# Optimization experiments

Measured on AMD Instinct MI355X. Metric: run time of the kernel, lower is better.

## Reference

```python
import jax, jax.numpy as jnp
import numpy as np

N = 100_000      # nodes
E = 1_600_000    # edges (avg degree 16)
F_IN = 128       # input features
H = 64           # hidden
C = 40           # classes


def setup_inputs() -> dict:
    key = jax.random.key(0)
    ks = jax.random.split(key, 12)
    s = 0.05
    return {
        "x": jax.random.normal(ks[0], (N, F_IN), dtype=jnp.float32),
        "edge_index": jax.random.randint(ks[1], (2, E), 0, N, dtype=jnp.int64),
        "edge_weight": jax.random.uniform(ks[2], (E,), dtype=jnp.float32),
        # first_lin: Linear(F_IN, H)
        "W_first": jax.random.normal(ks[3], (F_IN, H), dtype=jnp.float32) * s,
        "b_first": jnp.zeros((H,), jnp.float32),
        # convs[0], convs[1]: GCNConv(H, H)
        "W_c1": jax.random.normal(ks[4], (H, H), dtype=jnp.float32) * s,
        "b_c1": jnp.zeros((H,), jnp.float32),
        "W_c2": jax.random.normal(ks[5], (H, H), dtype=jnp.float32) * s,
        "b_c2": jnp.zeros((H,), jnp.float32),
        # lin2: Linear(H, C)
        "W_out": jax.random.normal(ks[6], (H, C), dtype=jnp.float32) * s,
        "b_out": jnp.zeros((C,), jnp.float32),
    }


def gcn_conv(h, edge_weight, row, col, W, b, n):
    """PyG GCNConv: h' = D^-1/2 (A + I) D^-1/2 (h W) + b, with edge weights."""
    h = h @ W                                        # [n, H]
    # add self-loops with weight 1
    loops = jnp.arange(n, dtype=row.dtype)
    row_sl = jnp.concatenate([row, loops])           # source nodes
    col_sl = jnp.concatenate([col, loops])           # target nodes
    ew_sl = jnp.concatenate([edge_weight, jnp.ones((n,), edge_weight.dtype)])
    # symmetric normalization
    deg = jax.ops.segment_sum(ew_sl, col_sl, num_segments=n)
    dinv = jnp.where(deg > 0, jax.lax.rsqrt(jnp.where(deg > 0, deg, 1.0)), 0.0)
    norm = dinv[row_sl] * ew_sl * dinv[col_sl]       # [E+n]
    # gather -> scale -> scatter-add at targets
    msgs = norm[:, None] * h[row_sl]                 # [E+n, H]
    out = jax.ops.segment_sum(msgs, col_sl, num_segments=n)
    return out + b


def reference(x, edge_index, edge_weight, W_first, b_first, W_c1, b_c1,
              W_c2, b_c2, W_out, b_out):
    row, col = edge_index[0], edge_index[1]
    n = x.shape[0]
    h = jax.nn.relu(x @ W_first + b_first)           # first_lin + relu (dropout eval no-op)
    h = jax.nn.relu(gcn_conv(h, edge_weight, row, col, W_c1, b_c1, n))
    h = jax.nn.relu(gcn_conv(h, edge_weight, row, col, W_c2, b_c2, n))
    logits = h @ W_out + b_out                       # lin2
    return jax.nn.log_softmax(logits, axis=-1)
```

## Files before the change

### kernel.cpp

```cpp
#include <hip/hip_runtime.h>
#include <hip/hip_bf16.h>
#include <cstdint>
#include <cstddef>

#define NN 100000
#define NE 1600000
#define FIN 128
#define HD 64
#define NC 40
#define NTILE (NN / 16)
#define MM_BLOCKS ((NTILE + 3) / 4)

#define BUK 256
#define NBUK ((NN + BUK - 1) / BUK)
#define EPB 1024
#define NBLK ((NE + EPB - 1) / EPB)

#define XSTR 68
#define HSTR 36

typedef unsigned short u16;
typedef unsigned int u32;
typedef __attribute__((ext_vector_type(8))) short short8v;
typedef __attribute__((ext_vector_type(4))) float accf4;
typedef __attribute__((ext_vector_type(2))) float f32x2;

__device__ __forceinline__ float u2lo(u32 u) { return __uint_as_float(u << 16); }
__device__ __forceinline__ float u2hi(u32 u) { return __uint_as_float(u & 0xFFFF0000u); }
__device__ __forceinline__ u16 f2b(float f) {
    u32 u = __float_as_uint(f);
    return (u16)((u + 0x7FFFu + ((u >> 16) & 1u)) >> 16);
}
__device__ __forceinline__ u32 pk2(float lo, float hi) {
    return (u32)f2b(lo) | ((u32)f2b(hi) << 16);
}
__device__ __forceinline__ unsigned char f2fp8(float v) {
    int r = __builtin_amdgcn_cvt_pk_fp8_f32(v, 0.f, 0, false);
    return (unsigned char)(r & 0xFF);
}

__launch_bounds__(256)
__global__ void k_build1(const int* __restrict__ ei, u32* __restrict__ hist,
                         const float* __restrict__ x, const float* __restrict__ W,
                         const float* __restrict__ b, u16* __restrict__ out) {
    if (blockIdx.x < NBLK) {
        __shared__ u32 lh[NBUK];
        int blk = blockIdx.x, tid = threadIdx.x;
        for (int i = tid; i < NBUK; i += 256) lh[i] = 0;
        __syncthreads();
        #pragma unroll
        for (int it = 0; it < EPB / 256; it++) {
            int e = blk * EPB + it * 256 + tid;
            if (e < NE) {
                int col = ei[NE + e];
                atomicAdd(&lh[col >> 8], 1u);
            }
        }
        __syncthreads();
        for (int i = tid; i < NBUK; i += 256)
            hist[(size_t)blk * NBUK + i] = lh[i];
        return;
    }
    __shared__ u32 xs[64 * XSTR];
    int tid = threadIdx.x;
    int bi  = blockIdx.x - NBLK;
    int nodeB = bi * 64;
    const float4* x4 = (const float4*)x;
    for (int idx = tid; idx < 64 * 16; idx += 256) {
        int row = idx >> 4, seg = idx & 15;
        uint4 d = make_uint4(0u, 0u, 0u, 0u);
        if (nodeB + row < NN) {
            float4 a = x4[(size_t)(nodeB + row) * 32 + seg * 2];
            float4 c = x4[(size_t)(nodeB + row) * 32 + seg * 2 + 1];
            d.x = pk2(a.x, a.y);
            d.y = pk2(a.z, a.w);
            d.z = pk2(c.x, c.y);
            d.w = pk2(c.z, c.w);
        }
        *(uint4*)(xs + row * XSTR + seg * 4) = d;
    }
    __syncthreads();
    int lane = tid & 63;
    int wv   = tid >> 6;
    int tile = bi * 4 + wv;
    if (tile >= NTILE) return;
    int row = lane & 15;
    int kg  = lane >> 4;
    short8v bW[4][4];
    #pragma unroll
    for (int kt = 0; kt < 4; kt++)
        #pragma unroll
        for (int ct = 0; ct < 4; ct++)
            #pragma unroll
            for (int j = 0; j < 8; j++)
                bW[kt][ct][j] = (short)f2b(W[(kt*32 + kg*8 + j) * HD + ct*16 + row]);
    int node0 = tile * 16;
    short8v af[4];
    #pragma unroll
    for (int kt = 0; kt < 4; kt++)
        af[kt] = *(const short8v*)(xs + (wv*16 + row) * XSTR + kt * 16 + kg * 4);
    accf4 acc[4] = {};
    #pragma unroll
    for (int kt = 0; kt < 4; kt++)
        #pragma unroll
        for (int ct = 0; ct < 4; ct++)
            acc[ct] = __builtin_amdgcn_mfma_f32_16x16x32_bf16(af[kt], bW[kt][ct], acc[ct], 0, 0, 0);
    #pragma unroll
    for (int ct = 0; ct < 4; ct++) {
        float bias = b[ct*16 + row];
        #pragma unroll
        for (int r = 0; r < 4; r++) {
            float v = fmaxf(acc[ct][r] + bias, 0.f);
            out[(size_t)(node0 + kg*4 + r) * HD + ct*16 + row] = f2b(v);
        }
    }
}

__global__ void k_bscan(u32* __restrict__ hist, u32* __restrict__ bucketTotal) {
    int b = blockIdx.x;
    int lane = threadIdx.x;
    u32 carry = 0;
    for (int j0 = 0; j0 < NBLK; j0 += 64) {
        int j = j0 + lane;
        u32 v = (j < NBLK) ? hist[(size_t)j * NBUK + b] : 0;
        u32 inc = v;
        #pragma unroll
        for (int d = 1; d < 64; d <<= 1) {
            u32 t = __shfl_up(inc, d);
            if (lane >= d) inc += t;
        }
        if (j < NBLK) hist[(size_t)j * NBUK + b] = carry + inc - v;
        carry += __shfl(inc, 63);
    }
    if (lane == 0) bucketTotal[b] = carry;
}

__global__ void k_bstart(const u32* __restrict__ bucketTotal, u32* __restrict__ bucketStart,
                         int* __restrict__ off) {
    int lane = threadIdx.x;
    u32 carry = 0;
    for (int j0 = 0; j0 < NBUK; j0 += 64) {
        int j = j0 + lane;
        u32 v = (j < NBUK) ? bucketTotal[j] : 0;
        u32 inc = v;
        #pragma unroll
        for (int d = 1; d < 64; d <<= 1) {
            u32 t = __shfl_up(inc, d);
            if (lane >= d) inc += t;
        }
        if (j < NBUK) bucketStart[j] = carry + inc - v;
        carry += __shfl(inc, 63);
    }
    if (lane == 0) { bucketStart[NBUK] = carry; off[NN] = (int)carry; }
}

__launch_bounds__(256)
__global__ void k_scatter(const int* __restrict__ ei, const float* __restrict__ ew,
                          const u32* __restrict__ hist, const u32* __restrict__ bucketStart,
                          uint2* __restrict__ rec) {
    __shared__ u32 lh[NBUK];
    __shared__ u32 gb[NBUK];
    int blk = blockIdx.x, tid = threadIdx.x;
    for (int i = tid; i < NBUK; i += 256) {
        lh[i] = 0;
        gb[i] = bucketStart[i] + hist[(size_t)blk * NBUK + i];
    }
    __syncthreads();
    #pragma unroll
    for (int it = 0; it < EPB / 256; it++) {
        int e = blk * EPB + it * 256 + tid;
        if (e < NE) {
            int row = ei[e], col = ei[NE + e];
            float wv = ew[e];
            int bkt = col >> 8;
            u32 cl = (u32)(col & 255);
            u32 r = atomicAdd(&lh[bkt], 1u);
            u32 slot = gb[bkt] + r;
            rec[slot] = make_uint2((u32)row | (cl << 24), __float_as_uint(wv));
        }
    }
}

__launch_bounds__(256)
__global__ void k_bucket(const uint2* __restrict__ rec, const u32* __restrict__ bucketStart,
                         float* __restrict__ dinv, int* __restrict__ off,
                         uint2* __restrict__ csr) {
    __shared__ u32 lpk[BUK];
    __shared__ u32 loff[BUK];
    __shared__ u32 wt[4];
    int b = blockIdx.x, tid = threadIdx.x;
    int base = b * BUK;
    u32 seg0 = bucketStart[b], seg1 = bucketStart[b + 1];
    int nb = (int)(seg1 - seg0);
    lpk[tid] = 0;
    __syncthreads();
    for (int idx = tid; idx < nb; idx += 256) {
        uint2 ab = rec[seg0 + idx];
        u32 cl = ab.x >> 24;
        u32 fx = __float2uint_rn(__uint_as_float(ab.y) * 16384.0f);
        atomicAdd(&lpk[cl], (1u << 20) | fx);
    }
    __syncthreads();
    u32 pk = lpk[tid];
    u32 cnt = pk >> 20;
    int node = base + tid;
    if (node < NN) dinv[node] = rsqrtf(1.0f + (float)(pk & 0xFFFFFu) * (1.0f / 16384.0f));
    int lane = tid & 63, wid = tid >> 6;
    u32 inc = cnt;
    #pragma unroll
    for (int d = 1; d < 64; d <<= 1) {
        u32 t = __shfl_up(inc, d);
        if (lane >= d) inc += t;
    }
    if (lane == 63) wt[wid] = inc;
    __syncthreads();
    u32 wof = 0;
    #pragma unroll
    for (int k = 0; k < 4; k++) if (k < wid) wof += wt[k];
    loff[tid] = wof + inc - cnt;
    if (node < NN) off[node] = (int)(seg0 + loff[tid]);
    lpk[tid] = 0;
    __syncthreads();
    for (int idx = tid; idx < nb; idx += 256) {
        uint2 ab = rec[seg0 + idx];
        u32 cl = ab.x >> 24;
        u32 r2 = atomicAdd(&lpk[cl], 1u);
        csr[seg0 + loff[cl] + r2] = make_uint2(ab.x & 0xFFFFFFu, ab.y);
    }
}

__launch_bounds__(256)
__global__ void k_mm64(const u16* __restrict__ A, const float* __restrict__ W,
                       const float* __restrict__ dinv, unsigned char* __restrict__ out) {
    int lane = threadIdx.x & 63;
    int tile = blockIdx.x * 4 + (threadIdx.x >> 6);
    if (tile >= NTILE) return;
    int row = lane & 15;
    int kg  = lane >> 4;
    short8v bW[2][4];
    #pragma unroll
    for (int kt = 0; kt < 2; kt++)
        #pragma unroll
        for (int ct = 0; ct < 4; ct++)
            #pragma unroll
            for (int j = 0; j < 8; j++)
                bW[kt][ct][j] = (short)f2b(W[(kt*32 + kg*8 + j) * HD + ct*16 + row]);
    int node0 = tile * 16;
    const u16* ar = A + (size_t)(node0 + row) * HD + kg * 8;
    short8v af0 = *(const short8v*)(ar);
    short8v af1 = *(const short8v*)(ar + 32);
    accf4 acc[4] = {};
    #pragma unroll
    for (int ct = 0; ct < 4; ct++) {
        acc[ct] = __builtin_amdgcn_mfma_f32_16x16x32_bf16(af0, bW[0][ct], acc[ct], 0, 0, 0);
        acc[ct] = __builtin_amdgcn_mfma_f32_16x16x32_bf16(af1, bW[1][ct], acc[ct], 0, 0, 0);
    }
    float dr[4];
    #pragma unroll
    for (int r = 0; r < 4; r++) dr[r] = dinv[node0 + kg*4 + r];
    #pragma unroll
    for (int ct = 0; ct < 4; ct++)
        #pragma unroll
        for (int r = 0; r < 4; r++)
            out[(size_t)(node0 + kg*4 + r) * HD + ct*16 + row] = f2fp8(acc[ct][r] * dr[r]);
}

__launch_bounds__(256)
__global__ void k_aggmm(const uint2* __restrict__ T8, const int* __restrict__ off,
                        const uint2* __restrict__ csr, const float* __restrict__ dinv,
                        const float* __restrict__ bias, const float* __restrict__ W2,
                        unsigned char* __restrict__ tbl2) {
    __shared__ u32 hs[32 * HSTR];
    int lane = threadIdx.x & 63;
    int wave = threadIdx.x >> 6;
    int g    = lane >> 3;
    int fp   = lane & 7;
    int node = blockIdx.x * 32 + wave * 8 + g;
    int s = off[node], e = off[node + 1];
    int deg = e - s;
    float di = dinv[node];
    float a0, a1, a2, a3, a4, a5, a6, a7;
    {
        uint2 sw = T8[(size_t)node * 8 + fp];
        f32x2 p0 = __builtin_amdgcn_cvt_pk_f32_fp8(sw.x, false);
        f32x2 p1 = __builtin_amdgcn_cvt_pk_f32_fp8(sw.x, true);
        f32x2 p2 = __builtin_amdgcn_cvt_pk_f32_fp8(sw.y, false);
        f32x2 p3 = __builtin_amdgcn_cvt_pk_f32_fp8(sw.y, true);
        a0 = p0[0]; a1 = p0[1]; a2 = p1[0]; a3 = p1[1];
        a4 = p2[0]; a5 = p2[1]; a6 = p3[0]; a7 = p3[1];
    }
    uint2 c0 = csr[s+0], c1 = csr[s+1], c2 = csr[s+2], c3 = csr[s+3];
    for (int j = 0; __any(j < deg); j += 4) {
        uint2 n0 = csr[s+j+4], n1 = csr[s+j+5], n2 = csr[s+j+6], n3 = csr[s+j+7];
        bool b0 = (j+0) < deg; u32 r0 = b0 ? c0.x : (u32)node; float w0 = b0 ? __uint_as_float(c0.y) : 0.f;
        bool b1 = (j+1) < deg; u32 r1 = b1 ? c1.x : (u32)node; float w1 = b1 ? __uint_as_float(c1.y) : 0.f;
        bool b2 = (j+2) < deg; u32 r2 = b2 ? c2.x : (u32)node; float w2 = b2 ? __uint_as_float(c2.y) : 0.f;
        bool b3 = (j+3) < deg; u32 r3 = b3 ? c3.x : (u32)node; float w3 = b3 ? __uint_as_float(c3.y) : 0.f;
        uint2 g0 = T8[(size_t)r0 * 8 + fp];
        uint2 g1 = T8[(size_t)r1 * 8 + fp];
        uint2 g2 = T8[(size_t)r2 * 8 + fp];
        uint2 g3 = T8[(size_t)r3 * 8 + fp];
        #pragma unroll
        for (int q = 0; q < 4; q++) {
            u32 lox = (q == 0) ? g0.x : (q == 1) ? g1.x : (q == 2) ? g2.x : g3.x;
            u32 loy = (q == 0) ? g0.y : (q == 1) ? g1.y : (q == 2) ? g2.y : g3.y;
            float wq = (q == 0) ? w0 : (q == 1) ? w1 : (q == 2) ? w2 : w3;
            f32x2 p0 = __builtin_amdgcn_cvt_pk_f32_fp8(lox, false);
            f32x2 p1 = __builtin_amdgcn_cvt_pk_f32_fp8(lox, true);
            f32x2 p2 = __builtin_amdgcn_cvt_pk_f32_fp8(loy, false);
            f32x2 p3 = __builtin_amdgcn_cvt_pk_f32_fp8(loy, true);
            a0 += wq * p0[0]; a1 += wq * p0[1];
            a2 += wq * p1[0]; a3 += wq * p1[1];
            a4 += wq * p2[0]; a5 += wq * p2[1];
            a6 += wq * p3[0]; a7 += wq * p3[1];
        }
        c0 = n0; c1 = n1; c2 = n2; c3 = n3;
    }
    float4 blo = *(const float4*)(bias + fp * 8);
    float4 bhi = *(const float4*)(bias + fp * 8 + 4);
    int lrow = wave * 8 + g;
    uint4 hv;
    hv.x = pk2(fmaxf(di*a0 + blo.x, 0.f), fmaxf(di*a1 + blo.y, 0.f));
    hv.y = pk2(fmaxf(di*a2 + blo.z, 0.f), fmaxf(di*a3 + blo.w, 0.f));
    hv.z = pk2(fmaxf(di*a4 + bhi.x, 0.f), fmaxf(di*a5 + bhi.y, 0.f));
    hv.w = pk2(fmaxf(di*a6 + bhi.z, 0.f), fmaxf(di*a7 + bhi.w, 0.f));
    *(uint4*)(hs + lrow * HSTR + fp * 4) = hv;
    __syncthreads();
    int row = lane & 15;
    int kg  = lane >> 4;
    int t      = wave & 1;
    int ctbase = (wave >> 1) * 2;
    short8v bW[2][2];
    #pragma unroll
    for (int kt = 0; kt < 2; kt++)
        #pragma unroll
        for (int cc = 0; cc < 2; cc++)
            #pragma unroll
            for (int j = 0; j < 8; j++)
                bW[kt][cc][j] = (short)f2b(W2[(kt*32 + kg*8 + j) * HD + (ctbase+cc)*16 + row]);
    short8v af0 = *(const short8v*)(hs + (t*16 + row) * HSTR + kg * 4);
    short8v af1 = *(const short8v*)(hs + (t*16 + row) * HSTR + 16 + kg * 4);
    accf4 acc[2] = {};
    #pragma unroll
    for (int cc = 0; cc < 2; cc++) {
        acc[cc] = __builtin_amdgcn_mfma_f32_16x16x32_bf16(af0, bW[0][cc], acc[cc], 0, 0, 0);
        acc[cc] = __builtin_amdgcn_mfma_f32_16x16x32_bf16(af1, bW[1][cc], acc[cc], 0, 0, 0);
    }
    int node0 = blockIdx.x * 32 + t * 16;
    float dr[4];
    #pragma unroll
    for (int r = 0; r < 4; r++) dr[r] = dinv[node0 + kg*4 + r];
    #pragma unroll
    for (int cc = 0; cc < 2; cc++)
        #pragma unroll
        for (int r = 0; r < 4; r++)
            tbl2[(size_t)(node0 + kg*4 + r) * HD + (ctbase+cc)*16 + row] = f2fp8(acc[cc][r] * dr[r]);
}

__launch_bounds__(256)
__global__ void k_aggout(const uint2* __restrict__ T8, const int* __restrict__ off,
                         const uint2* __restrict__ csr, const float* __restrict__ dinv,
                         const float* __restrict__ bias, const float* __restrict__ Wo,
                         const float* __restrict__ bo, float* __restrict__ outp) {
    __shared__ u32 hs[32 * HSTR];
    int lane = threadIdx.x & 63;
    int wave = threadIdx.x >> 6;
    int g    = lane >> 3;
    int fp   = lane & 7;
    int node = blockIdx.x * 32 + wave * 8 + g;
    int s = off[node], e = off[node + 1];
    int deg = e - s;
    float di = dinv[node];
    float a0, a1, a2, a3, a4, a5, a6, a7;
    {
        uint2 sw = T8[(size_t)node * 8 + fp];
        f32x2 p0 = __builtin_amdgcn_cvt_pk_f32_fp8(sw.x, false);
        f32x2 p1 = __builtin_amdgcn_cvt_pk_f32_fp8(sw.x, true);
        f32x2 p2 = __builtin_amdgcn_cvt_pk_f32_fp8(sw.y, false);
        f32x2 p3 = __builtin_amdgcn_cvt_pk_f32_fp8(sw.y, true);
        a0 = p0[0]; a1 = p0[1]; a2 = p1[0]; a3 = p1[1];
        a4 = p2[0]; a5 = p2[1]; a6 = p3[0]; a7 = p3[1];
    }
    uint2 c0 = csr[s+0], c1 = csr[s+1], c2 = csr[s+2], c3 = csr[s+3];
    for (int j = 0; __any(j < deg); j += 4) {
        uint2 n0 = csr[s+j+4], n1 = csr[s+j+5], n2 = csr[s+j+6], n3 = csr[s+j+7];
        bool b0 = (j+0) < deg; u32 r0 = b0 ? c0.x : (u32)node; float w0 = b0 ? __uint_as_float(c0.y) : 0.f;
        bool b1 = (j+1) < deg; u32 r1 = b1 ? c1.x : (u32)node; float w1 = b1 ? __uint_as_float(c1.y) : 0.f;
        bool b2 = (j+2) < deg; u32 r2 = b2 ? c2.x : (u32)node; float w2 = b2 ? __uint_as_float(c2.y) : 0.f;
        bool b3 = (j+3) < deg; u32 r3 = b3 ? c3.x : (u32)node; float w3 = b3 ? __uint_as_float(c3.y) : 0.f;
        uint2 g0 = T8[(size_t)r0 * 8 + fp];
        uint2 g1 = T8[(size_t)r1 * 8 + fp];
        uint2 g2 = T8[(size_t)r2 * 8 + fp];
        uint2 g3 = T8[(size_t)r3 * 8 + fp];
        #pragma unroll
        for (int q = 0; q < 4; q++) {
            u32 lox = (q == 0) ? g0.x : (q == 1) ? g1.x : (q == 2) ? g2.x : g3.x;
            u32 loy = (q == 0) ? g0.y : (q == 1) ? g1.y : (q == 2) ? g2.y : g3.y;
            float wq = (q == 0) ? w0 : (q == 1) ? w1 : (q == 2) ? w2 : w3;
            f32x2 p0 = __builtin_amdgcn_cvt_pk_f32_fp8(lox, false);
            f32x2 p1 = __builtin_amdgcn_cvt_pk_f32_fp8(lox, true);
            f32x2 p2 = __builtin_amdgcn_cvt_pk_f32_fp8(loy, false);
            f32x2 p3 = __builtin_amdgcn_cvt_pk_f32_fp8(loy, true);
            a0 += wq * p0[0]; a1 += wq * p0[1];
            a2 += wq * p1[0]; a3 += wq * p1[1];
            a4 += wq * p2[0]; a5 += wq * p2[1];
            a6 += wq * p3[0]; a7 += wq * p3[1];
        }
        c0 = n0; c1 = n1; c2 = n2; c3 = n3;
    }
    float4 blo = *(const float4*)(bias + fp * 8);
    float4 bhi = *(const float4*)(bias + fp * 8 + 4);
    int lrow = wave * 8 + g;
    uint4 hv;
    hv.x = pk2(fmaxf(di*a0 + blo.x, 0.f), fmaxf(di*a1 + blo.y, 0.f));
    hv.y = pk2(fmaxf(di*a2 + blo.z, 0.f), fmaxf(di*a3 + blo.w, 0.f));
    hv.z = pk2(fmaxf(di*a4 + bhi.x, 0.f), fmaxf(di*a5 + bhi.y, 0.f));
    hv.w = pk2(fmaxf(di*a6 + bhi.z, 0.f), fmaxf(di*a7 + bhi.w, 0.f));
    *(uint4*)(hs + lrow * HSTR + fp * 4) = hv;
    __syncthreads();
    if (wave >= 2) return;
    int row = lane & 15;
    int kg  = lane >> 4;
    int t = wave;
    short8v bW[2][3];
    #pragma unroll
    for (int kt = 0; kt < 2; kt++)
        #pragma unroll
        for (int ct = 0; ct < 3; ct++) {
            int col = ct*16 + row;
            #pragma unroll
            for (int j = 0; j < 8; j++)
                bW[kt][ct][j] = (col < NC) ? (short)f2b(Wo[(kt*32 + kg*8 + j) * NC + col]) : (short)0;
        }
    short8v af0 = *(const short8v*)(hs + (t*16 + row) * HSTR + kg * 4);
    short8v af1 = *(const short8v*)(hs + (t*16 + row) * HSTR + 16 + kg * 4);
    accf4 acc[3] = {};
    #pragma unroll
    for (int ct = 0; ct < 3; ct++) {
        acc[ct] = __builtin_amdgcn_mfma_f32_16x16x32_bf16(af0, bW[0][ct], acc[ct], 0, 0, 0);
        acc[ct] = __builtin_amdgcn_mfma_f32_16x16x32_bf16(af1, bW[1][ct], acc[ct], 0, 0, 0);
    }
    int node0 = blockIdx.x * 32 + t * 16;
    float bias0 = bo[row];
    float bias1 = bo[16 + row];
    bool  has2  = (32 + row) < NC;
    float bias2 = has2 ? bo[32 + row] : 0.f;
    #pragma unroll
    for (int r = 0; r < 4; r++) {
        float l0 = acc[0][r] + bias0;
        float l1 = acc[1][r] + bias1;
        float l2 = has2 ? acc[2][r] + bias2 : -1e30f;
        float m = fmaxf(fmaxf(l0, l1), l2);
        #pragma unroll
        for (int s2 = 8; s2 > 0; s2 >>= 1) m = fmaxf(m, __shfl_xor(m, s2));
        float sum = expf(l0 - m) + expf(l1 - m) + (has2 ? expf(l2 - m) : 0.f);
        #pragma unroll
        for (int s2 = 8; s2 > 0; s2 >>= 1) sum += __shfl_xor(sum, s2);
        float ls = logf(sum);
        size_t base = (size_t)(node0 + kg*4 + r) * NC;
        outp[base + row]      = (l0 - m) - ls;
        outp[base + 16 + row] = (l1 - m) - ls;
        if (has2) outp[base + 32 + row] = (l2 - m) - ls;
    }
}


extern "C" void kernel_launch(void* const* d_in, const int* in_sizes, int n_in,
                              void* d_out, int out_size, void* d_ws, size_t ws_size,
                              hipStream_t stream) {
    const float* x   = (const float*)d_in[0];
    const int*   ei  = (const int*)  d_in[1];
    const float* ew  = (const float*)d_in[2];
    const float* Wf  = (const float*)d_in[3];
    const float* bf  = (const float*)d_in[4];
    const float* Wc1 = (const float*)d_in[5];
    const float* bc1 = (const float*)d_in[6];
    const float* Wc2 = (const float*)d_in[7];
    const float* bc2 = (const float*)d_in[8];
    const float* Wo  = (const float*)d_in[9];
    const float* bo  = (const float*)d_in[10];
    float* out = (float*)d_out;

    char* w = (char*)d_ws;
    auto alloc = [&](size_t bytes) {
        char* p = w;
        w += (bytes + 511) & ~(size_t)511;
        return p;
    };
    u32*   hist = (u32*)  alloc((size_t)NBLK * NBUK * 4);
    u32*   btot = (u32*)  alloc((size_t)NBUK * 4);
    u32*   bst  = (u32*)  alloc((size_t)(NBUK + 1) * 4);
    float* dinv = (float*)alloc((size_t)NN * 4);
    int*   off  = (int*)  alloc((size_t)(NN + 1) * 4);
    uint2* rec  = (uint2*)alloc((size_t)NE * 8);
    uint2* csr  = (uint2*)alloc((size_t)(NE + 128) * 8);
    u16*   hA   = (u16*)  alloc((size_t)NN * HD * 2);
    u16*   hB   = (u16*)  alloc((size_t)NN * HD * 2);

    k_build1 <<<NBLK + MM_BLOCKS, 256, 0, stream>>>(ei, hist, x, Wf, bf, hA);
    k_bscan  <<<NBUK, 64, 0, stream>>>(hist, btot);
    k_bstart <<<1, 64, 0, stream>>>(btot, bst, off);
    k_scatter<<<NBLK, 256, 0, stream>>>(ei, ew, hist, bst, rec);
    k_bucket <<<NBUK, 256, 0, stream>>>(rec, bst, dinv, off, csr);

    k_mm64  <<<MM_BLOCKS, 256, 0, stream>>>(hA, Wc1, dinv, (unsigned char*)hB);
    k_aggmm <<<NN / 32, 256, 0, stream>>>((const uint2*)hB, off, csr, dinv, bc1, Wc2,
                                          (unsigned char*)hA);
    k_aggout<<<NN / 32, 256, 0, stream>>>((const uint2*)hA, off, csr, dinv, bc2, Wo, bo, out);
}
```

Baseline: 156.1 us.

## Partition CSR neighbors by source half and gather each half in separate passes

Each node's CSR neighbor list is reordered so that sources with index below N/2 come first, with a per-node count stored in a new nlo array. The aggregation kernels run the gather loop twice, once per half, so that across a wave the gathered feature rows tend to come from one half of the table at a time, which is meant to improve cache locality. In exchange it adds extra shared-memory atomics in the bucket kernel, a second loop with its own tail padding and prefetch per node, and an extra array read.

```diff
diff --git a/kernel.cpp b/kernel.cpp
--- a/kernel.cpp
+++ b/kernel.cpp
@@ -10,6 +10,7 @@
 #define NC 40
 #define NTILE (NN / 16)
 #define MM_BLOCKS ((NTILE + 3) / 4)
+#define NHALF (NN / 2)
 
 #define BUK 256
 #define NBUK ((NN + BUK - 1) / BUK)
@@ -184,27 +185,35 @@
 __launch_bounds__(256)
 __global__ void k_bucket(const uint2* __restrict__ rec, const u32* __restrict__ bucketStart,
                          float* __restrict__ dinv, int* __restrict__ off,
-                         uint2* __restrict__ csr) {
+                         u16* __restrict__ nlo, uint2* __restrict__ csr) {
     __shared__ u32 lpk[BUK];
     __shared__ u32 loff[BUK];
+    __shared__ u32 nlo_s[BUK];
+    __shared__ u32 rankhi[BUK];
     __shared__ u32 wt[4];
     int b = blockIdx.x, tid = threadIdx.x;
     int base = b * BUK;
     u32 seg0 = bucketStart[b], seg1 = bucketStart[b + 1];
     int nb = (int)(seg1 - seg0);
     lpk[tid] = 0;
+    nlo_s[tid] = 0;
     __syncthreads();
     for (int idx = tid; idx < nb; idx += 256) {
         uint2 ab = rec[seg0 + idx];
         u32 cl = ab.x >> 24;
+        u32 rw = ab.x & 0xFFFFFFu;
         u32 fx = __float2uint_rn(__uint_as_float(ab.y) * 16384.0f);
         atomicAdd(&lpk[cl], (1u << 20) | fx);
+        if (rw < NHALF) atomicAdd(&nlo_s[cl], 1u);
     }
     __syncthreads();
     u32 pk = lpk[tid];
     u32 cnt = pk >> 20;
     int node = base + tid;
-    if (node < NN) dinv[node] = rsqrtf(1.0f + (float)(pk & 0xFFFFFu) * (1.0f / 16384.0f));
+    if (node < NN) {
+        dinv[node] = rsqrtf(1.0f + (float)(pk & 0xFFFFFu) * (1.0f / 16384.0f));
+        nlo[node] = (u16)nlo_s[tid];
+    }
     int lane = tid & 63, wid = tid >> 6;
     u32 inc = cnt;
     #pragma unroll
@@ -220,12 +229,21 @@
     loff[tid] = wof + inc - cnt;
     if (node < NN) off[node] = (int)(seg0 + loff[tid]);
     lpk[tid] = 0;
+    rankhi[tid] = 0;
     __syncthreads();
     for (int idx = tid; idx < nb; idx += 256) {
         uint2 ab = rec[seg0 + idx];
         u32 cl = ab.x >> 24;
-        u32 r2 = atomicAdd(&lpk[cl], 1u);
-        csr[seg0 + loff[cl] + r2] = make_uint2(ab.x & 0xFFFFFFu, ab.y);
+        u32 rw = ab.x & 0xFFFFFFu;
+        u32 slot;
+        if (rw < NHALF) {
+            u32 r2 = atomicAdd(&lpk[cl], 1u);
+            slot = seg0 + loff[cl] + r2;
+        } else {
+            u32 r2 = atomicAdd(&rankhi[cl], 1u);
+            slot = seg0 + loff[cl] + nlo_s[cl] + r2;
+        }
+        csr[slot] = make_uint2(rw, ab.y);
     }
 }
 
@@ -268,8 +286,8 @@
 __launch_bounds__(256)
 __global__ void k_aggmm(const uint2* __restrict__ T8, const int* __restrict__ off,
                         const uint2* __restrict__ csr, const float* __restrict__ dinv,
-                        const float* __restrict__ bias, const float* __restrict__ W2,
-                        unsigned char* __restrict__ tbl2) {
+                        const u16* __restrict__ nlo, const float* __restrict__ bias,
+                        const float* __restrict__ W2, unsigned char* __restrict__ tbl2) {
     __shared__ u32 hs[32 * HSTR];
     int lane = threadIdx.x & 63;
     int wave = threadIdx.x >> 6;
@@ -277,7 +295,7 @@
     int fp   = lane & 7;
     int node = blockIdx.x * 32 + wave * 8 + g;
     int s = off[node], e = off[node + 1];
-    int deg = e - s;
+    int mid = s + (int)nlo[node];
     float di = dinv[node];
     float a0, a1, a2, a3, a4, a5, a6, a7;
     {
@@ -289,33 +307,38 @@
         a0 = p0[0]; a1 = p0[1]; a2 = p1[0]; a3 = p1[1];
         a4 = p2[0]; a5 = p2[1]; a6 = p3[0]; a7 = p3[1];
     }
-    uint2 c0 = csr[s+0], c1 = csr[s+1], c2 = csr[s+2], c3 = csr[s+3];
-    for (int j = 0; __any(j < deg); j += 4) {
-        uint2 n0 = csr[s+j+4], n1 = csr[s+j+5], n2 = csr[s+j+6], n3 = csr[s+j+7];
-        bool b0 = (j+0) < deg; u32 r0 = b0 ? c0.x : (u32)node; float w0 = b0 ? __uint_as_float(c0.y) : 0.f;
-        bool b1 = (j+1) < deg; u32 r1 = b1 ? c1.x : (u32)node; float w1 = b1 ? __uint_as_float(c1.y) : 0.f;
-        bool b2 = (j+2) < deg; u32 r2 = b2 ? c2.x : (u32)node; float w2 = b2 ? __uint_as_float(c2.y) : 0.f;
-        bool b3 = (j+3) < deg; u32 r3 = b3 ? c3.x : (u32)node; float w3 = b3 ? __uint_as_float(c3.y) : 0.f;
-        uint2 g0 = T8[(size_t)r0 * 8 + fp];
-        uint2 g1 = T8[(size_t)r1 * 8 + fp];
-        uint2 g2 = T8[(size_t)r2 * 8 + fp];
-        uint2 g3 = T8[(size_t)r3 * 8 + fp];
-        #pragma unroll
-        for (int q = 0; q < 4; q++) {
-            u32 lox = (q == 0) ? g0.x : (q == 1) ? g1.x : (q == 2) ? g2.x : g3.x;
-            u32 loy = (q == 0) ? g0.y : (q == 1) ? g1.y : (q == 2) ? g2.y : g3.y;
-            float wq = (q == 0) ? w0 : (q == 1) ? w1 : (q == 2) ? w2 : w3;
-            f32x2 p0 = __builtin_amdgcn_cvt_pk_f32_fp8(lox, false);
-            f32x2 p1 = __builtin_amdgcn_cvt_pk_f32_fp8(lox, true);
-            f32x2 p2 = __builtin_amdgcn_cvt_pk_f32_fp8(loy, false);
-            f32x2 p3 = __builtin_amdgcn_cvt_pk_f32_fp8(loy, true);
-            a0 += wq * p0[0]; a1 += wq * p0[1];
-            a2 += wq * p1[0]; a3 += wq * p1[1];
-            a4 += wq * p2[0]; a5 += wq * p2[1];
-            a6 += wq * p3[0]; a7 += wq * p3[1];
-        }
-        c0 = n0; c1 = n1; c2 = n2; c3 = n3;
-    }
+    auto gather = [&](int lo, int hi) {
+        int len = hi - lo;
+        uint2 c0 = csr[lo+0], c1 = csr[lo+1], c2 = csr[lo+2], c3 = csr[lo+3];
+        for (int j = 0; __any(j < len); j += 4) {
+            uint2 n0 = csr[lo+j+4], n1 = csr[lo+j+5], n2 = csr[lo+j+6], n3 = csr[lo+j+7];
+            bool b0 = (j+0) < len; u32 r0 = b0 ? c0.x : (u32)node; float w0 = b0 ? __uint_as_float(c0.y) : 0.f;
+            bool b1 = (j+1) < len; u32 r1 = b1 ? c1.x : (u32)node; float w1 = b1 ? __uint_as_float(c1.y) : 0.f;
+            bool b2 = (j+2) < len; u32 r2 = b2 ? c2.x : (u32)node; float w2 = b2 ? __uint_as_float(c2.y) : 0.f;
+            bool b3 = (j+3) < len; u32 r3 = b3 ? c3.x : (u32)node; float w3 = b3 ? __uint_as_float(c3.y) : 0.f;
+            uint2 g0 = T8[(size_t)r0 * 8 + fp];
+            uint2 g1 = T8[(size_t)r1 * 8 + fp];
+            uint2 g2 = T8[(size_t)r2 * 8 + fp];
+            uint2 g3 = T8[(size_t)r3 * 8 + fp];
+            #pragma unroll
+            for (int q = 0; q < 4; q++) {
+                u32 lox = (q == 0) ? g0.x : (q == 1) ? g1.x : (q == 2) ? g2.x : g3.x;
+                u32 loy = (q == 0) ? g0.y : (q == 1) ? g1.y : (q == 2) ? g2.y : g3.y;
+                float wq = (q == 0) ? w0 : (q == 1) ? w1 : (q == 2) ? w2 : w3;
+                f32x2 p0 = __builtin_amdgcn_cvt_pk_f32_fp8(lox, false);
+                f32x2 p1 = __builtin_amdgcn_cvt_pk_f32_fp8(lox, true);
+                f32x2 p2 = __builtin_amdgcn_cvt_pk_f32_fp8(loy, false);
+                f32x2 p3 = __builtin_amdgcn_cvt_pk_f32_fp8(loy, true);
+                a0 += wq * p0[0]; a1 += wq * p0[1];
+                a2 += wq * p1[0]; a3 += wq * p1[1];
+                a4 += wq * p2[0]; a5 += wq * p2[1];
+                a6 += wq * p3[0]; a7 += wq * p3[1];
+            }
+            c0 = n0; c1 = n1; c2 = n2; c3 = n3;
+        }
+    };
+    gather(s, mid);
+    gather(mid, e);
     float4 blo = *(const float4*)(bias + fp * 8);
     float4 bhi = *(const float4*)(bias + fp * 8 + 4);
     int lrow = wave * 8 + g;
@@ -360,8 +383,9 @@
 __launch_bounds__(256)
 __global__ void k_aggout(const uint2* __restrict__ T8, const int* __restrict__ off,
                          const uint2* __restrict__ csr, const float* __restrict__ dinv,
-                         const float* __restrict__ bias, const float* __restrict__ Wo,
-                         const float* __restrict__ bo, float* __restrict__ outp) {
+                         const u16* __restrict__ nlo, const float* __restrict__ bias,
+                         const float* __restrict__ Wo, const float* __restrict__ bo,
+                         float* __restrict__ outp) {
     __shared__ u32 hs[32 * HSTR];
     int lane = threadIdx.x & 63;
     int wave = threadIdx.x >> 6;
@@ -369,7 +393,7 @@
     int fp   = lane & 7;
     int node = blockIdx.x * 32 + wave * 8 + g;
     int s = off[node], e = off[node + 1];
-    int deg = e - s;
+    int mid = s + (int)nlo[node];
     float di = dinv[node];
     float a0, a1, a2, a3, a4, a5, a6, a7;
     {
@@ -381,33 +405,38 @@
         a0 = p0[0]; a1 = p0[1]; a2 = p1[0]; a3 = p1[1];
         a4 = p2[0]; a5 = p2[1]; a6 = p3[0]; a7 = p3[1];
     }
-    uint2 c0 = csr[s+0], c1 = csr[s+1], c2 = csr[s+2], c3 = csr[s+3];
-    for (int j = 0; __any(j < deg); j += 4) {
-        uint2 n0 = csr[s+j+4], n1 = csr[s+j+5], n2 = csr[s+j+6], n3 = csr[s+j+7];
-        bool b0 = (j+0) < deg; u32 r0 = b0 ? c0.x : (u32)node; float w0 = b0 ? __uint_as_float(c0.y) : 0.f;
-        bool b1 = (j+1) < deg; u32 r1 = b1 ? c1.x : (u32)node; float w1 = b1 ? __uint_as_float(c1.y) : 0.f;
-        bool b2 = (j+2) < deg; u32 r2 = b2 ? c2.x : (u32)node; float w2 = b2 ? __uint_as_float(c2.y) : 0.f;
-        bool b3 = (j+3) < deg; u32 r3 = b3 ? c3.x : (u32)node; float w3 = b3 ? __uint_as_float(c3.y) : 0.f;
-        uint2 g0 = T8[(size_t)r0 * 8 + fp];
-        uint2 g1 = T8[(size_t)r1 * 8 + fp];
-        uint2 g2 = T8[(size_t)r2 * 8 + fp];
-        uint2 g3 = T8[(size_t)r3 * 8 + fp];
-        #pragma unroll
-        for (int q = 0; q < 4; q++) {
-            u32 lox = (q == 0) ? g0.x : (q == 1) ? g1.x : (q == 2) ? g2.x : g3.x;
-            u32 loy = (q == 0) ? g0.y : (q == 1) ? g1.y : (q == 2) ? g2.y : g3.y;
-            float wq = (q == 0) ? w0 : (q == 1) ? w1 : (q == 2) ? w2 : w3;
-            f32x2 p0 = __builtin_amdgcn_cvt_pk_f32_fp8(lox, false);
-            f32x2 p1 = __builtin_amdgcn_cvt_pk_f32_fp8(lox, true);
-            f32x2 p2 = __builtin_amdgcn_cvt_pk_f32_fp8(loy, false);
-            f32x2 p3 = __builtin_amdgcn_cvt_pk_f32_fp8(loy, true);
-            a0 += wq * p0[0]; a1 += wq * p0[1];
-            a2 += wq * p1[0]; a3 += wq * p1[1];
-            a4 += wq * p2[0]; a5 += wq * p2[1];
-            a6 += wq * p3[0]; a7 += wq * p3[1];
-        }
-        c0 = n0; c1 = n1; c2 = n2; c3 = n3;
-    }
+    auto gather = [&](int lo, int hi) {
+        int len = hi - lo;
+        uint2 c0 = csr[lo+0], c1 = csr[lo+1], c2 = csr[lo+2], c3 = csr[lo+3];
+        for (int j = 0; __any(j < len); j += 4) {
+            uint2 n0 = csr[lo+j+4], n1 = csr[lo+j+5], n2 = csr[lo+j+6], n3 = csr[lo+j+7];
+            bool b0 = (j+0) < len; u32 r0 = b0 ? c0.x : (u32)node; float w0 = b0 ? __uint_as_float(c0.y) : 0.f;
+            bool b1 = (j+1) < len; u32 r1 = b1 ? c1.x : (u32)node; float w1 = b1 ? __uint_as_float(c1.y) : 0.f;
+            bool b2 = (j+2) < len; u32 r2 = b2 ? c2.x : (u32)node; float w2 = b2 ? __uint_as_float(c2.y) : 0.f;
+            bool b3 = (j+3) < len; u32 r3 = b3 ? c3.x : (u32)node; float w3 = b3 ? __uint_as_float(c3.y) : 0.f;
+            uint2 g0 = T8[(size_t)r0 * 8 + fp];
+            uint2 g1 = T8[(size_t)r1 * 8 + fp];
+            uint2 g2 = T8[(size_t)r2 * 8 + fp];
+            uint2 g3 = T8[(size_t)r3 * 8 + fp];
+            #pragma unroll
+            for (int q = 0; q < 4; q++) {
+                u32 lox = (q == 0) ? g0.x : (q == 1) ? g1.x : (q == 2) ? g2.x : g3.x;
+                u32 loy = (q == 0) ? g0.y : (q == 1) ? g1.y : (q == 2) ? g2.y : g3.y;
+                float wq = (q == 0) ? w0 : (q == 1) ? w1 : (q == 2) ? w2 : w3;
+                f32x2 p0 = __builtin_amdgcn_cvt_pk_f32_fp8(lox, false);
+                f32x2 p1 = __builtin_amdgcn_cvt_pk_f32_fp8(lox, true);
+                f32x2 p2 = __builtin_amdgcn_cvt_pk_f32_fp8(loy, false);
+                f32x2 p3 = __builtin_amdgcn_cvt_pk_f32_fp8(loy, true);
+                a0 += wq * p0[0]; a1 += wq * p0[1];
+                a2 += wq * p1[0]; a3 += wq * p1[1];
+                a4 += wq * p2[0]; a5 += wq * p2[1];
+                a6 += wq * p3[0]; a7 += wq * p3[1];
+            }
+            c0 = n0; c1 = n1; c2 = n2; c3 = n3;
+        }
+    };
+    gather(s, mid);
+    gather(mid, e);
     float4 blo = *(const float4*)(bias + fp * 8);
     float4 bhi = *(const float4*)(bias + fp * 8 + 4);
     int lrow = wave * 8 + g;
@@ -492,6 +521,7 @@
     u32*   bst  = (u32*)  alloc((size_t)(NBUK + 1) * 4);
     float* dinv = (float*)alloc((size_t)NN * 4);
     int*   off  = (int*)  alloc((size_t)(NN + 1) * 4);
+    u16*   nlo  = (u16*)  alloc((size_t)NN * 2);
     uint2* rec  = (uint2*)alloc((size_t)NE * 8);
     uint2* csr  = (uint2*)alloc((size_t)(NE + 128) * 8);
     u16*   hA   = (u16*)  alloc((size_t)NN * HD * 2);
@@ -501,10 +531,10 @@
     k_bscan  <<<NBUK, 64, 0, stream>>>(hist, btot);
     k_bstart <<<1, 64, 0, stream>>>(btot, bst, off);
     k_scatter<<<NBLK, 256, 0, stream>>>(ei, ew, hist, bst, rec);
-    k_bucket <<<NBUK, 256, 0, stream>>>(rec, bst, dinv, off, csr);
+    k_bucket <<<NBUK, 256, 0, stream>>>(rec, bst, dinv, off, nlo, csr);
 
     k_mm64  <<<MM_BLOCKS, 256, 0, stream>>>(hA, Wc1, dinv, (unsigned char*)hB);
-    k_aggmm <<<NN / 32, 256, 0, stream>>>((const uint2*)hB, off, csr, dinv, bc1, Wc2,
+    k_aggmm <<<NN / 32, 256, 0, stream>>>((const uint2*)hB, off, csr, dinv, nlo, bc1, Wc2,
                                           (unsigned char*)hA);
-    k_aggout<<<NN / 32, 256, 0, stream>>>((const uint2*)hA, off, csr, dinv, bc2, Wo, bo, out);
-}
+    k_aggout<<<NN / 32, 256, 0, stream>>>((const uint2*)hA, off, csr, dinv, nlo, bc2, Wo, bo, out);
+}
```

After: 158.1 us. Within noise of the previous version (+1.3%).
